# Kernel tuning notes

Measured on AMD Instinct MI355X. Metric: run time of the kernel, lower is better.

Reference implementation:

```python
import jax, jax.numpy as jnp
import numpy as np

B, S, D_IN, D_OUT = 4, 4096, 4096, 4096

def setup_inputs() -> dict:
    key = jax.random.key(0)
    k1, k2, k3, k4 = jax.random.split(key, 4)
    x = jax.random.normal(k1, (B, S, D_IN), dtype=jnp.float32)
    weight_q = jax.random.randint(k2, (D_OUT, D_IN), 0, 127, dtype=jnp.int32)
    scale = jax.random.uniform(k3, (1,), dtype=jnp.float32) * 0.01 + 1e-4
    bias = jax.random.normal(k4, (D_OUT,), dtype=jnp.float32)
    return {"x": x, "weight_q": weight_q, "scale": scale, "bias": bias}

def reference(x, weight_q, scale, bias):
    # dequantize: int weight * per-tensor scale -> fp32 weight [D_OUT, D_IN]
    weight = weight_q.astype(jnp.float32) * scale[0]
    # linear: y = x @ W^T + b  -> [B, S, D_OUT]
    return jnp.einsum('bsd,od->bso', x, weight) + bias
```

## Files before the change

### kernel.cpp

```cpp
#include <hip/hip_runtime.h>
#include <stdint.h>

constexpr int M = 16384;
constexpr int N = 4096;
constexpr int K = 4096;
constexpr int BM = 256, BN = 256, BKB = 128;
constexpr int NT = K / BKB;

typedef __attribute__((ext_vector_type(4))) int i32x4;

__global__ __launch_bounds__(256) void quant_x_kernel(
    const float* __restrict__ x, signed char* __restrict__ o,
    float* __restrict__ row_step) {
    const int wave = threadIdx.x >> 6;
    const int lane = threadIdx.x & 63;
    const int row  = blockIdx.x * 4 + wave;
    const float4* xr = (const float4*)(x + (size_t)row * K);

    float4 v[16];
#pragma unroll
    for (int i = 0; i < 16; i++) v[i] = xr[lane + 64 * i];

    float amax = 0.f;
#pragma unroll
    for (int i = 0; i < 16; i++)
        amax = fmaxf(amax,
               fmaxf(fmaxf(fabsf(v[i].x), fabsf(v[i].y)),
                     fmaxf(fabsf(v[i].z), fabsf(v[i].w))));
#pragma unroll
    for (int off = 32; off > 0; off >>= 1)
        amax = fmaxf(amax, __shfl_xor(amax, off, 64));

    const float inv = (amax > 0.f) ? 127.0f / amax : 0.f;
    if (lane == 0) row_step[row] = (amax > 0.f) ? amax / 127.0f : 0.f;

    char4* orow = (char4*)(o + (size_t)row * K);
#pragma unroll
    for (int i = 0; i < 16; i++) {
        char4 r;
        r.x = (signed char)__float2int_rn(v[i].x * inv);
        r.y = (signed char)__float2int_rn(v[i].y * inv);
        r.z = (signed char)__float2int_rn(v[i].z * inv);
        r.w = (signed char)__float2int_rn(v[i].w * inv);
        orow[lane + 64 * i] = r;
    }
}

__global__ __launch_bounds__(256) void quant_w_kernel(
    const int* __restrict__ q, signed char* __restrict__ o) {
    const size_t base = (size_t)blockIdx.x * 256 + threadIdx.x;
    const int4* qv = (const int4*)q + base * 4;
    int4 v0 = qv[0], v1 = qv[1], v2 = qv[2], v3 = qv[3];
#define PACK(v) (int)((unsigned)((v).x & 255) | ((unsigned)((v).y & 255) << 8) | \
                      ((unsigned)((v).z & 255) << 16) | ((unsigned)((v).w & 255) << 24))
    int4 r;
    r.x = PACK(v0); r.y = PACK(v1); r.z = PACK(v2); r.w = PACK(v3);
#undef PACK
    ((int4*)o)[base] = r;
}

__global__ __launch_bounds__(512, 2) void gemm_i8_kernel(
    const signed char* __restrict__ A,
    const signed char* __restrict__ B,
    const float* __restrict__ row_step,
    const float* __restrict__ scale,
    const float* __restrict__ bias,
    float* __restrict__ C) {
    __shared__ __align__(16) signed char As[2 * BM * BKB];
    __shared__ __align__(16) signed char Bs[2 * BN * BKB];

    const int t    = threadIdx.x;
    const int lane = t & 63;
    const int wave = t >> 6;
    const int wr   = wave >> 2;
    const int wc   = wave & 3;
    const int r16  = lane & 15;
    const int quad = lane >> 4;

    const int xcd   = blockIdx.x & 7;
    const int local = blockIdx.x >> 3;
    const int sg    = local >> 5;
    const int u     = local & 31;
    const int bm = (xcd >> 1) * 16 + (sg >> 1) * 8 + (u >> 2);
    const int bn = (xcd & 1) * 8 + (sg & 1) * 4 + (u & 3);
    const int mBase = bm * BM;
    const int nBase = bn * BN;

    const int sr   = t >> 3;
    const int scol = ((t & 7) ^ (sr & 7)) << 4;

    typedef __attribute__((address_space(3))) signed char* lds_p;
    typedef const __attribute__((address_space(1))) signed char* g_p;

    const g_p AgS = (g_p)(A + (size_t)(mBase + sr) * K + scol);
    const g_p BgS = (g_p)(B + (size_t)(nBase + sr) * K + scol);

#define STAGE_A(bofs, h, kt) do {                                            \
    __builtin_amdgcn_global_load_lds(                                        \
        AgS + (size_t)((h) * 128) * K + (size_t)(kt) * BKB,                  \
        (lds_p)(As + (bofs) + ((h) << 14) + t * 16), 16, 0, 0);              \
    __builtin_amdgcn_global_load_lds(                                        \
        AgS + (size_t)((h) * 128 + 64) * K + (size_t)(kt) * BKB,             \
        (lds_p)(As + (bofs) + ((h) << 14) + 8192 + t * 16), 16, 0, 0);       \
  } while (0)
#define STAGE_B(bofs, h, kt) do {                                            \
    __builtin_amdgcn_global_load_lds(                                        \
        BgS + (size_t)((h) * 128) * K + (size_t)(kt) * BKB,                  \
        (lds_p)(Bs + (bofs) + ((h) << 14) + t * 16), 16, 0, 0);              \
    __builtin_amdgcn_global_load_lds(                                        \
        BgS + (size_t)((h) * 128 + 64) * K + (size_t)(kt) * BKB,             \
        (lds_p)(Bs + (bofs) + ((h) << 14) + 8192 + t * 16), 16, 0, 0);       \
  } while (0)

    int aoff[8], boff[4], csw[2];
#pragma unroll
    for (int m = 0; m < 8; ++m) aoff[m] = (wr * 128 + m * 16 + r16) * BKB;
#pragma unroll
    for (int n = 0; n < 4; ++n) boff[n] = (wc * 64 + n * 16 + r16) * BKB;
    csw[0] = ((0 + quad) ^ (r16 & 7)) << 4;
    csw[1] = ((4 + quad) ^ (r16 & 7)) << 4;

    i32x4 acc[8][4];
    const i32x4 zero = {0, 0, 0, 0};
#pragma unroll
    for (int m = 0; m < 8; ++m)
#pragma unroll
        for (int n = 0; n < 4; ++n) acc[m][n] = zero;

    STAGE_B(0, 0, 0);
    STAGE_B(0, 1, 0);
    STAGE_A(0, 0, 0);
    STAGE_A(0, 1, 0);
    STAGE_B(1 << 15, 0, 1);
    STAGE_B(1 << 15, 1, 1);
    asm volatile("s_waitcnt vmcnt(4)" ::: "memory");
    __builtin_amdgcn_s_barrier();

    i32x4 bv[4][2];

    for (int kt = 0; kt < NT; ++kt) {
        const int bO = (kt & 1) << 15;
        const int bX = bO ^ (1 << 15);
#pragma unroll
        for (int p = 0; p < 4; ++p) {
            const i32x4 a00 = *(const i32x4*)(As + bO + aoff[2 * p] + csw[0]);
            const i32x4 a01 = *(const i32x4*)(As + bO + aoff[2 * p] + csw[1]);
            const i32x4 a10 = *(const i32x4*)(As + bO + aoff[2 * p + 1] + csw[0]);
            const i32x4 a11 = *(const i32x4*)(As + bO + aoff[2 * p + 1] + csw[1]);
            if (p == 0) {
#pragma unroll
                for (int n = 0; n < 4; ++n) {
                    bv[n][0] = *(const i32x4*)(Bs + bO + boff[n] + csw[0]);
                    bv[n][1] = *(const i32x4*)(Bs + bO + boff[n] + csw[1]);
                }
            }
            if (p == 0 && kt + 1 < NT) STAGE_A(bX, 0, kt + 1);
            if (p == 1 && kt + 1 < NT) STAGE_A(bX, 1, kt + 1);
            if (p == 2 && kt + 2 < NT) STAGE_B(bO, 0, kt + 2);
            if (p == 3) {
                if (kt + 2 < NT) STAGE_B(bO, 1, kt + 2);
                if (kt < NT - 2) {
                    asm volatile("s_waitcnt vmcnt(4)" ::: "memory");
                } else if (kt == NT - 2) {
                    asm volatile("s_waitcnt vmcnt(0)" ::: "memory");
                }
            }
            __builtin_amdgcn_s_barrier();
            __builtin_amdgcn_s_setprio(1);
#pragma unroll
            for (int ks = 0; ks < 2; ++ks) {
                const i32x4 x0 = ks ? a01 : a00;
                const i32x4 x1 = ks ? a11 : a10;
#pragma unroll
                for (int n = 0; n < 4; ++n) {
                    acc[2 * p][n] = __builtin_amdgcn_mfma_i32_16x16x64_i8(
                        x0, bv[n][ks], acc[2 * p][n], 0, 0, 0);
                    acc[2 * p + 1][n] = __builtin_amdgcn_mfma_i32_16x16x64_i8(
                        x1, bv[n][ks], acc[2 * p + 1][n], 0, 0, 0);
                }
            }
            __builtin_amdgcn_s_setprio(0);
            __builtin_amdgcn_s_barrier();
        }
    }

    const float s0 = scale[0];
    float bvals[4];
#pragma unroll
    for (int n = 0; n < 4; ++n)
        bvals[n] = bias[nBase + wc * 64 + n * 16 + r16];
    float rsv[8][4];
#pragma unroll
    for (int m = 0; m < 8; ++m)
#pragma unroll
        for (int r = 0; r < 4; ++r)
            rsv[m][r] = row_step[mBase + wr * 128 + m * 16 + quad * 4 + r] * s0;

#pragma unroll
    for (int m = 0; m < 8; ++m) {
#pragma unroll
        for (int n = 0; n < 4; ++n) {
            const int col = nBase + wc * 64 + n * 16 + r16;
#pragma unroll
            for (int r = 0; r < 4; ++r) {
                const int row = mBase + wr * 128 + m * 16 + quad * 4 + r;
                C[(size_t)row * N + col] =
                    (float)acc[m][n][r] * rsv[m][r] + bvals[n];
            }
        }
    }
#undef STAGE_A
#undef STAGE_B
}

extern "C" void kernel_launch(void* const* d_in, const int* in_sizes, int n_in,
                              void* d_out, int out_size, void* d_ws, size_t ws_size,
                              hipStream_t stream) {
    const float* x     = (const float*)d_in[0];
    const int*   wq    = (const int*)d_in[1];
    const float* scale = (const float*)d_in[2];
    const float* bias  = (const float*)d_in[3];
    float*       out   = (float*)d_out;

    float*       rs = (float*)d_ws;
    signed char* xb = (signed char*)(rs + M);
    signed char* wb = xb + (size_t)M * K;

    quant_x_kernel<<<M / 4, 256, 0, stream>>>(x, xb, rs);
    quant_w_kernel<<<(int)((size_t)N * K / 16 / 256), 256, 0, stream>>>(wq, wb);

    constexpr int NWG = (M / BM) * (N / BN);
    gemm_i8_kernel<<<NWG, 512, 0, stream>>>(xb, wb, rs, scale, bias, out);
}
```

Baseline: 762.6 us.

## Switch GEMM to 32x32x32 int8 MFMA and merge quantization kernels

The int8 GEMM inner loop now uses 32x32x32 MFMA tiles (4x2 per wave) in place of 16x16x64 tiles (8x4 per wave). The LDS fragment loads and the epilogue row/column mapping are reworked to match the 32x32 accumulator layout. This cuts the number of MFMA issues and LDS fragment reads per K step, at the cost of changing the register layout and the output store pattern. Separately, the x and weight quantization kernels are merged into one launch by splitting on block index, saving one kernel launch.

```diff
diff --git a/kernel.cpp b/kernel.cpp
--- a/kernel.cpp
+++ b/kernel.cpp
@@ -8,55 +8,56 @@
 constexpr int NT = K / BKB;
 
 typedef __attribute__((ext_vector_type(4))) int i32x4;
-
-__global__ __launch_bounds__(256) void quant_x_kernel(
-    const float* __restrict__ x, signed char* __restrict__ o,
+typedef __attribute__((ext_vector_type(16))) int i32x16;
+
+__global__ __launch_bounds__(256) void quant_kernel(
+    const float* __restrict__ x, const int* __restrict__ wq,
+    signed char* __restrict__ xo, signed char* __restrict__ wo,
     float* __restrict__ row_step) {
-    const int wave = threadIdx.x >> 6;
-    const int lane = threadIdx.x & 63;
-    const int row  = blockIdx.x * 4 + wave;
-    const float4* xr = (const float4*)(x + (size_t)row * K);
-
-    float4 v[16];
-#pragma unroll
-    for (int i = 0; i < 16; i++) v[i] = xr[lane + 64 * i];
-
-    float amax = 0.f;
-#pragma unroll
-    for (int i = 0; i < 16; i++)
-        amax = fmaxf(amax,
-               fmaxf(fmaxf(fabsf(v[i].x), fabsf(v[i].y)),
-                     fmaxf(fabsf(v[i].z), fabsf(v[i].w))));
-#pragma unroll
-    for (int off = 32; off > 0; off >>= 1)
-        amax = fmaxf(amax, __shfl_xor(amax, off, 64));
-
-    const float inv = (amax > 0.f) ? 127.0f / amax : 0.f;
-    if (lane == 0) row_step[row] = (amax > 0.f) ? amax / 127.0f : 0.f;
-
-    char4* orow = (char4*)(o + (size_t)row * K);
-#pragma unroll
-    for (int i = 0; i < 16; i++) {
-        char4 r;
-        r.x = (signed char)__float2int_rn(v[i].x * inv);
-        r.y = (signed char)__float2int_rn(v[i].y * inv);
-        r.z = (signed char)__float2int_rn(v[i].z * inv);
-        r.w = (signed char)__float2int_rn(v[i].w * inv);
-        orow[lane + 64 * i] = r;
-    }
-}
-
-__global__ __launch_bounds__(256) void quant_w_kernel(
-    const int* __restrict__ q, signed char* __restrict__ o) {
-    const size_t base = (size_t)blockIdx.x * 256 + threadIdx.x;
-    const int4* qv = (const int4*)q + base * 4;
-    int4 v0 = qv[0], v1 = qv[1], v2 = qv[2], v3 = qv[3];
+    if (blockIdx.x < M / 4) {
+        const int wave = threadIdx.x >> 6;
+        const int lane = threadIdx.x & 63;
+        const int row  = blockIdx.x * 4 + wave;
+        const float4* xr = (const float4*)(x + (size_t)row * K);
+
+        float4 v[16];
+#pragma unroll
+        for (int i = 0; i < 16; i++) v[i] = xr[lane + 64 * i];
+
+        float amax = 0.f;
+#pragma unroll
+        for (int i = 0; i < 16; i++)
+            amax = fmaxf(amax,
+                   fmaxf(fmaxf(fabsf(v[i].x), fabsf(v[i].y)),
+                         fmaxf(fabsf(v[i].z), fabsf(v[i].w))));
+#pragma unroll
+        for (int off = 32; off > 0; off >>= 1)
+            amax = fmaxf(amax, __shfl_xor(amax, off, 64));
+
+        const float inv = (amax > 0.f) ? 127.0f / amax : 0.f;
+        if (lane == 0) row_step[row] = (amax > 0.f) ? amax / 127.0f : 0.f;
+
+        char4* orow = (char4*)(xo + (size_t)row * K);
+#pragma unroll
+        for (int i = 0; i < 16; i++) {
+            char4 r;
+            r.x = (signed char)__float2int_rn(v[i].x * inv);
+            r.y = (signed char)__float2int_rn(v[i].y * inv);
+            r.z = (signed char)__float2int_rn(v[i].z * inv);
+            r.w = (signed char)__float2int_rn(v[i].w * inv);
+            orow[lane + 64 * i] = r;
+        }
+    } else {
+        const size_t base = (size_t)(blockIdx.x - M / 4) * 256 + threadIdx.x;
+        const int4* qv = (const int4*)wq + base * 4;
+        int4 v0 = qv[0], v1 = qv[1], v2 = qv[2], v3 = qv[3];
 #define PACK(v) (int)((unsigned)((v).x & 255) | ((unsigned)((v).y & 255) << 8) | \
                       ((unsigned)((v).z & 255) << 16) | ((unsigned)((v).w & 255) << 24))
-    int4 r;
-    r.x = PACK(v0); r.y = PACK(v1); r.z = PACK(v2); r.w = PACK(v3);
+        int4 r;
+        r.x = PACK(v0); r.y = PACK(v1); r.z = PACK(v2); r.w = PACK(v3);
 #undef PACK
-    ((int4*)o)[base] = r;
+        ((int4*)wo)[base] = r;
+    }
 }
 
 __global__ __launch_bounds__(512, 2) void gemm_i8_kernel(
@@ -69,13 +70,13 @@
     __shared__ __align__(16) signed char As[2 * BM * BKB];
     __shared__ __align__(16) signed char Bs[2 * BN * BKB];
 
-    const int t    = threadIdx.x;
-    const int lane = t & 63;
-    const int wave = t >> 6;
-    const int wr   = wave >> 2;
-    const int wc   = wave & 3;
-    const int r16  = lane & 15;
-    const int quad = lane >> 4;
+    const int t     = threadIdx.x;
+    const int lane  = t & 63;
+    const int wave  = t >> 6;
+    const int wr    = wave >> 2;
+    const int wc    = wave & 3;
+    const int l31   = lane & 31;
+    const int khalf = lane >> 5;
 
     const int xcd   = blockIdx.x & 7;
     const int local = blockIdx.x >> 3;
@@ -112,20 +113,22 @@
         (lds_p)(Bs + (bofs) + ((h) << 14) + 8192 + t * 16), 16, 0, 0);       \
   } while (0)
 
-    int aoff[8], boff[4], csw[2];
-#pragma unroll
-    for (int m = 0; m < 8; ++m) aoff[m] = (wr * 128 + m * 16 + r16) * BKB;
-#pragma unroll
-    for (int n = 0; n < 4; ++n) boff[n] = (wc * 64 + n * 16 + r16) * BKB;
-    csw[0] = ((0 + quad) ^ (r16 & 7)) << 4;
-    csw[1] = ((4 + quad) ^ (r16 & 7)) << 4;
-
-    i32x4 acc[8][4];
-    const i32x4 zero = {0, 0, 0, 0};
-#pragma unroll
-    for (int m = 0; m < 8; ++m)
-#pragma unroll
-        for (int n = 0; n < 4; ++n) acc[m][n] = zero;
+    int aoff[4], boff[2], csw[4];
+#pragma unroll
+    for (int mi = 0; mi < 4; ++mi) aoff[mi] = (wr * 128 + mi * 32 + l31) * BKB;
+#pragma unroll
+    for (int ni = 0; ni < 2; ++ni) boff[ni] = (wc * 64 + ni * 32 + l31) * BKB;
+#pragma unroll
+    for (int ks = 0; ks < 4; ++ks)
+        csw[ks] = ((ks * 2 + khalf) ^ (lane & 7)) << 4;
+
+    i32x16 acc[4][2];
+#pragma unroll
+    for (int mi = 0; mi < 4; ++mi)
+#pragma unroll
+        for (int ni = 0; ni < 2; ++ni)
+#pragma unroll
+            for (int r = 0; r < 16; ++r) acc[mi][ni][r] = 0;
 
     STAGE_B(0, 0, 0);
     STAGE_B(0, 1, 0);
@@ -136,23 +139,23 @@
     asm volatile("s_waitcnt vmcnt(4)" ::: "memory");
     __builtin_amdgcn_s_barrier();
 
-    i32x4 bv[4][2];
+    i32x4 bv[2][4];
 
     for (int kt = 0; kt < NT; ++kt) {
         const int bO = (kt & 1) << 15;
         const int bX = bO ^ (1 << 15);
 #pragma unroll
         for (int p = 0; p < 4; ++p) {
-            const i32x4 a00 = *(const i32x4*)(As + bO + aoff[2 * p] + csw[0]);
-            const i32x4 a01 = *(const i32x4*)(As + bO + aoff[2 * p] + csw[1]);
-            const i32x4 a10 = *(const i32x4*)(As + bO + aoff[2 * p + 1] + csw[0]);
-            const i32x4 a11 = *(const i32x4*)(As + bO + aoff[2 * p + 1] + csw[1]);
+            i32x4 av[4];
+#pragma unroll
+            for (int mi = 0; mi < 4; ++mi)
+                av[mi] = *(const i32x4*)(As + bO + aoff[mi] + csw[p]);
             if (p == 0) {
 #pragma unroll
-                for (int n = 0; n < 4; ++n) {
-                    bv[n][0] = *(const i32x4*)(Bs + bO + boff[n] + csw[0]);
-                    bv[n][1] = *(const i32x4*)(Bs + bO + boff[n] + csw[1]);
-                }
+                for (int ni = 0; ni < 2; ++ni)
+#pragma unroll
+                    for (int ks = 0; ks < 4; ++ks)
+                        bv[ni][ks] = *(const i32x4*)(Bs + bO + boff[ni] + csw[ks]);
             }
             if (p == 0 && kt + 1 < NT) STAGE_A(bX, 0, kt + 1);
             if (p == 1 && kt + 1 < NT) STAGE_A(bX, 1, kt + 1);
@@ -168,44 +171,37 @@
             __builtin_amdgcn_s_barrier();
             __builtin_amdgcn_s_setprio(1);
 #pragma unroll
-            for (int ks = 0; ks < 2; ++ks) {
-                const i32x4 x0 = ks ? a01 : a00;
-                const i32x4 x1 = ks ? a11 : a10;
-#pragma unroll
-                for (int n = 0; n < 4; ++n) {
-                    acc[2 * p][n] = __builtin_amdgcn_mfma_i32_16x16x64_i8(
-                        x0, bv[n][ks], acc[2 * p][n], 0, 0, 0);
-                    acc[2 * p + 1][n] = __builtin_amdgcn_mfma_i32_16x16x64_i8(
-                        x1, bv[n][ks], acc[2 * p + 1][n], 0, 0, 0);
-                }
-            }
+            for (int mi = 0; mi < 4; ++mi)
+#pragma unroll
+                for (int ni = 0; ni < 2; ++ni)
+                    acc[mi][ni] = __builtin_amdgcn_mfma_i32_32x32x32_i8(
+                        av[mi], bv[ni][p], acc[mi][ni], 0, 0, 0);
             __builtin_amdgcn_s_setprio(0);
             __builtin_amdgcn_s_barrier();
         }
     }
 
     const float s0 = scale[0];
-    float bvals[4];
-#pragma unroll
-    for (int n = 0; n < 4; ++n)
-        bvals[n] = bias[nBase + wc * 64 + n * 16 + r16];
-    float rsv[8][4];
-#pragma unroll
-    for (int m = 0; m < 8; ++m)
-#pragma unroll
-        for (int r = 0; r < 4; ++r)
-            rsv[m][r] = row_step[mBase + wr * 128 + m * 16 + quad * 4 + r] * s0;
-
-#pragma unroll
-    for (int m = 0; m < 8; ++m) {
-#pragma unroll
-        for (int n = 0; n < 4; ++n) {
-            const int col = nBase + wc * 64 + n * 16 + r16;
-#pragma unroll
-            for (int r = 0; r < 4; ++r) {
-                const int row = mBase + wr * 128 + m * 16 + quad * 4 + r;
+    float bvals[2];
+#pragma unroll
+    for (int ni = 0; ni < 2; ++ni)
+        bvals[ni] = bias[nBase + wc * 64 + ni * 32 + l31];
+
+#pragma unroll
+    for (int mi = 0; mi < 4; ++mi) {
+        const int rbase = mBase + wr * 128 + mi * 32 + 4 * khalf;
+        float rsv[16];
+#pragma unroll
+        for (int r = 0; r < 16; ++r)
+            rsv[r] = row_step[rbase + (r & 3) + 8 * (r >> 2)] * s0;
+#pragma unroll
+        for (int ni = 0; ni < 2; ++ni) {
+            const int col = nBase + wc * 64 + ni * 32 + l31;
+#pragma unroll
+            for (int r = 0; r < 16; ++r) {
+                const int row = rbase + (r & 3) + 8 * (r >> 2);
                 C[(size_t)row * N + col] =
-                    (float)acc[m][n][r] * rsv[m][r] + bvals[n];
+                    (float)acc[mi][ni][r] * rsv[r] + bvals[ni];
             }
         }
     }
@@ -226,8 +222,8 @@
     signed char* xb = (signed char*)(rs + M);
     signed char* wb = xb + (size_t)M * K;
 
-    quant_x_kernel<<<M / 4, 256, 0, stream>>>(x, xb, rs);
-    quant_w_kernel<<<(int)((size_t)N * K / 16 / 256), 256, 0, stream>>>(wq, wb);
+    quant_kernel<<<M / 4 + (int)((size_t)N * K / 16 / 256), 256, 0, stream>>>(
+        x, wq, xb, wb, rs);
 
     constexpr int NWG = (M / BM) * (N / BN);
     gemm_i8_kernel<<<NWG, 512, 0, stream>>>(xb, wb, rs, scale, bias, out);
```

New measurement: 759.4 us. No clear change (-0.4%).
